# Optimization experiments

Measured on AMD Instinct MI355X. Metric: run time of the kernel, lower is better.

The kernel has to match this reference:

```python
import jax, jax.numpy as jnp
import numpy as np

BOX_W, GIOU_W, OBJ_W, CLS_W, CTR_W = 5.0, 2.0, 1.0, 1.5, 0.5
POS_RADIUS = 1.0


def _bce_logits(x, t):
    # numerically stable binary cross entropy with logits
    return jnp.maximum(x, 0.0) - x * t + jnp.log1p(jnp.exp(-jnp.abs(x)))


def _focal(logits, targets, alpha=0.25, gamma=2.0):
    p = jax.nn.sigmoid(logits)
    ce = _bce_logits(logits, targets)
    p_t = p * targets + (1.0 - p) * (1.0 - targets)
    a_t = alpha * targets + (1.0 - alpha) * (1.0 - targets)
    return (a_t * ce * (1.0 - p_t) ** gamma).mean()


def _centerness(ltrb):
    l, t, r, b = ltrb[..., 0], ltrb[..., 1], ltrb[..., 2], ltrb[..., 3]
    hor = jnp.minimum(l, r) / jnp.maximum(jnp.maximum(l, r), 1e-6)
    ver = jnp.minimum(t, b) / jnp.maximum(jnp.maximum(t, b), 1e-6)
    return jnp.sqrt(jnp.maximum(hor * ver, 0.0))


def _build_targets(locations, gt_boxes, gt_labels, grid_h, grid_w, num_classes):
    # Vectorized equivalent of the sequential smallest-area-first assignment:
    # each location takes the smallest-area gt among its candidate gts.
    lx, ly = locations[:, 0], locations[:, 1]            # [L]
    cx, cy, w, h = (gt_boxes[..., i] for i in range(4))  # [B,M]
    x1, y1, x2, y2 = cx - w / 2, cy - h / 2, cx + w / 2, cy + h / 2
    area = w * h                                          # [B,M]
    # [B,M,L] booleans
    inside_box = (lx > x1[..., None]) & (ly > y1[..., None]) & (lx < x2[..., None]) & (ly < y2[..., None])
    rx, ry = POS_RADIUS / grid_w, POS_RADIUS / grid_h
    inside_center = (jnp.abs(lx - cx[..., None]) <= rx) & (jnp.abs(ly - cy[..., None]) <= ry)
    candidate = inside_box & inside_center
    # fallback: objects with no candidate grab the closest location (prefer inside-box)
    dist = (lx - cx[..., None]) ** 2 + (ly - cy[..., None]) ** 2
    dist_in = jnp.where(inside_box, dist, jnp.inf)
    best = jnp.where(inside_box.any(-1), jnp.argmin(dist_in, -1), jnp.argmin(dist, -1))  # [B,M]
    L = lx.shape[0]
    fallback = jax.nn.one_hot(best, L, dtype=bool)
    candidate = jnp.where(candidate.any(-1, keepdims=True), candidate, fallback)
    # per-location: pick candidate gt with min area (first index on ties)
    cost = jnp.where(candidate, area[..., None], jnp.inf)   # [B,M,L]
    assigned = jnp.argmin(cost, axis=1)                      # [B,L]
    positive = jnp.isfinite(jnp.min(cost, axis=1))           # [B,L]
    gt_xyxy = jnp.stack([x1, y1, x2, y2], axis=-1)           # [B,M,4]
    abox = jnp.take_along_axis(gt_xyxy, assigned[:, :, None], axis=1)  # [B,L,4]
    ltrb = jnp.stack([lx - abox[..., 0], ly - abox[..., 1], abox[..., 2] - lx, abox[..., 3] - ly], axis=-1)
    ltrb = jnp.maximum(ltrb, 1e-6)
    pos_f = positive.astype(jnp.float32)
    alab = jnp.take_along_axis(gt_labels, assigned, axis=1)  # [B,L]
    cls_t = jax.nn.one_hot(alab, num_classes, dtype=jnp.float32) * pos_f[..., None]
    ctr_t = _centerness(ltrb) * pos_f
    return abox * pos_f[..., None], ltrb * pos_f[..., None], cls_t, pos_f, ctr_t, positive


def _detection_loss(boxes_xyxy, box_deltas, class_logits, objectness, centerness,
                    locations, gt_boxes, gt_labels, grid_h, grid_w):
    C = class_logits.shape[-1]
    box_t, ltrb_t, cls_t, obj_t, ctr_t, positive = _build_targets(
        locations, gt_boxes, gt_labels, grid_h, grid_w, C)
    loss_obj = _focal(objectness, obj_t)
    loss_cls = _focal(class_logits, cls_t)
    # positive-weighted box terms (masked weighted sums over the full grid)
    weights = jnp.where(positive, jnp.maximum(jax.lax.stop_gradient(ctr_t), 0.1), 0.0)  # [B,L]
    wsum = weights.sum()
    # smooth L1 on ltrb deltas, beta=0.1
    beta = 0.1
    d = jnp.abs(box_deltas - ltrb_t)
    l1 = jnp.where(d < beta, 0.5 * d * d / beta, d - 0.5 * beta).mean(-1)  # [B,L]
    loss_l1 = (l1 * weights).sum() / wsum
    # elementwise GIoU between predicted and assigned gt xyxy boxes
    p, g = boxes_xyxy, box_t
    inter_lt = jnp.maximum(p[..., :2], g[..., :2])
    inter_rb = jnp.minimum(p[..., 2:], g[..., 2:])
    inter_wh = jnp.maximum(inter_rb - inter_lt, 0.0)
    inter = inter_wh[..., 0] * inter_wh[..., 1]
    area_p = jnp.maximum(p[..., 2] - p[..., 0], 0.0) * jnp.maximum(p[..., 3] - p[..., 1], 0.0)
    area_g = jnp.maximum(g[..., 2] - g[..., 0], 0.0) * jnp.maximum(g[..., 3] - g[..., 1], 0.0)
    union = area_p + area_g - inter
    iou = inter / jnp.maximum(union, 1e-6)
    hull_lt = jnp.minimum(p[..., :2], g[..., :2])
    hull_rb = jnp.maximum(p[..., 2:], g[..., 2:])
    hull_wh = jnp.maximum(hull_rb - hull_lt, 0.0)
    hull = hull_wh[..., 0] * hull_wh[..., 1]
    giou = iou - (hull - union) / jnp.maximum(hull, 1e-6)
    loss_giou = ((1.0 - giou) * weights).sum() / wsum
    ctr_bce = _bce_logits(centerness, ctr_t)
    loss_ctr = (ctr_bce * weights).sum() / wsum
    return (OBJ_W * loss_obj + CTR_W * loss_ctr + CLS_W * loss_cls
            + BOX_W * loss_l1 + GIOU_W * loss_giou)


def setup_inputs() -> dict:
    key = jax.random.key(0)
    ks = jax.random.split(key, 8)
    B, M, H, W, C = 16, 32, 128, 128, 80
    L = H * W
    ys, xs = jnp.meshgrid(jnp.arange(H, dtype=jnp.float32), jnp.arange(W, dtype=jnp.float32), indexing='ij')
    locations = jnp.stack([(xs + 0.5) / W, (ys + 0.5) / H], axis=-1).reshape(L, 2)
    gt_c = jax.random.uniform(ks[0], (B, M, 2), minval=0.1, maxval=0.9)
    gt_wh = jax.random.uniform(ks[1], (B, M, 2), minval=0.02, maxval=0.3)
    gt_boxes = jnp.concatenate([gt_c, gt_wh], axis=-1)
    gt_labels = jax.random.randint(ks[2], (B, M), 0, C)
    pc = jax.random.uniform(ks[3], (B, L, 2), minval=0.05, maxval=0.95)
    pwh = jax.random.uniform(ks[4], (B, L, 2), minval=0.02, maxval=0.3)
    boxes_xyxy = jnp.concatenate([pc - pwh / 2, pc + pwh / 2], axis=-1)
    box_deltas = jax.random.uniform(ks[5], (B, L, 4), minval=1e-3, maxval=0.3)
    class_logits = jax.random.normal(ks[6], (B, L, C), dtype=jnp.float32)
    k7, k8 = jax.random.split(ks[7])
    objectness = jax.random.normal(k7, (B, L), dtype=jnp.float32)
    centerness = jax.random.normal(k8, (B, L), dtype=jnp.float32)
    return {"boxes_xyxy": boxes_xyxy, "box_deltas": box_deltas, "class_logits": class_logits,
            "objectness": objectness, "centerness": centerness, "locations": locations,
            "gt_boxes": gt_boxes, "gt_labels": gt_labels, "grid_h": H, "grid_w": W}


def reference(boxes_xyxy, box_deltas, class_logits, objectness, centerness,
              locations, gt_boxes, gt_labels, grid_h, grid_w):
    return _detection_loss(boxes_xyxy, box_deltas, class_logits, objectness, centerness,
                           locations, gt_boxes, gt_labels, grid_h, grid_w)
```

## Files before the change

### kernel.cpp

```cpp
#include <hip/hip_runtime.h>
#include <cstdint>
#include <cstddef>
#include <math.h>

#define BOX_W_C  5.0f
#define GIOU_W_C 2.0f
#define OBJ_W_C  1.0f
#define CLS_W_C  1.5f
#define CTR_W_C  0.5f
#define POS_RADIUS_C 1.0f
#define MAXM 128
#define CLS_BLOCKS 2048

__device__ __forceinline__ float focal_elem(float x, float t) {
    float ax = fabsf(x);
    float e  = __expf(-ax);
    float lg = __logf(1.0f + e);
    float ce = fmaxf(x, 0.0f) - x * t + lg;
    float p  = (x >= 0.0f) ? (1.0f / (1.0f + e)) : (e / (1.0f + e));
    float p_t = p * t + (1.0f - p) * (1.0f - t);
    float a_t = 0.25f * t + 0.75f * (1.0f - t);
    float om  = 1.0f - p_t;
    return a_t * ce * om * om;
}

__global__ void gt_assign_kernel(const float* __restrict__ locations,
                                 const float* __restrict__ gt_boxes,
                                 const int* __restrict__ gh_p,
                                 const int* __restrict__ gw_p,
                                 int L, int M,
                                 float* __restrict__ info,
                                 int* __restrict__ flags) {
    int bm  = blockIdx.x;
    int tid = threadIdx.x;

    const float* gb = gt_boxes + (size_t)bm * 4;
    float cx = gb[0], cy = gb[1], w = gb[2], h = gb[3];
    float x1 = cx - w * 0.5f, y1 = cy - h * 0.5f;
    float x2 = cx + w * 0.5f, y2 = cy + h * 0.5f;
    float area = w * h;
    float rx = POS_RADIUS_C / (float)gw_p[0];
    float ry = POS_RADIUS_C / (float)gh_p[0];

    float bin_v  = INFINITY; int bin_i  = 0x7fffffff;
    float ball_v = INFINITY; int ball_i = 0x7fffffff;
    int any_cand = 0, any_in = 0;

    const float2* loc2 = (const float2*)locations;
    for (int l = tid; l < L; l += blockDim.x) {
        float2 p2 = loc2[l];
        float lx = p2.x, ly = p2.y;
        bool inb = (lx > x1) && (ly > y1) && (lx < x2) && (ly < y2);
        bool inc = (fabsf(lx - cx) <= rx) && (fabsf(ly - cy) <= ry);
        any_cand |= (int)(inb && inc);
        any_in   |= (int)inb;
        float dx = lx - cx, dy = ly - cy;
        float dist = dx * dx + dy * dy;
        if (dist < ball_v) { ball_v = dist; ball_i = l; }
        float din = inb ? dist : INFINITY;
        if (din < bin_v) { bin_v = din; bin_i = l; }
    }

    __shared__ float s_v1[512]; __shared__ int s_i1[512];
    __shared__ float s_v2[512]; __shared__ int s_i2[512];
    __shared__ int s_c[512]; __shared__ int s_n[512];
    s_v1[tid] = bin_v;  s_i1[tid] = bin_i;
    s_v2[tid] = ball_v; s_i2[tid] = ball_i;
    s_c[tid] = any_cand; s_n[tid] = any_in;
    __syncthreads();
    for (int s = blockDim.x / 2; s > 0; s >>= 1) {
        if (tid < s) {
            if (s_v1[tid + s] < s_v1[tid] ||
                (s_v1[tid + s] == s_v1[tid] && s_i1[tid + s] < s_i1[tid])) {
                s_v1[tid] = s_v1[tid + s]; s_i1[tid] = s_i1[tid + s];
            }
            if (s_v2[tid + s] < s_v2[tid] ||
                (s_v2[tid + s] == s_v2[tid] && s_i2[tid + s] < s_i2[tid])) {
                s_v2[tid] = s_v2[tid + s]; s_i2[tid] = s_i2[tid + s];
            }
            s_c[tid] |= s_c[tid + s];
            s_n[tid] |= s_n[tid + s];
        }
        __syncthreads();
    }
    if (tid == 0) {
        int best = s_n[0] ? s_i1[0] : s_i2[0];
        flags[bm * 2]     = s_c[0];
        flags[bm * 2 + 1] = best;
        float* oi = info + (size_t)bm * 8;
        oi[0] = x1; oi[1] = y1; oi[2] = x2; oi[3] = y2;
        oi[4] = cx; oi[5] = cy; oi[6] = area; oi[7] = 0.0f;
    }
}

__global__ void assign_loss_kernel(const float* __restrict__ boxes_xyxy,
                                   const float* __restrict__ box_deltas,
                                   const float* __restrict__ objectness,
                                   const float* __restrict__ centerness,
                                   const float* __restrict__ locations,
                                   const int* __restrict__ gt_labels,
                                   const int* __restrict__ gh_p,
                                   const int* __restrict__ gw_p,
                                   int L, int M, int bpb, int nblk,
                                   const float* __restrict__ info,
                                   const int* __restrict__ flags,
                                   short* __restrict__ lab_out,
                                   float* __restrict__ partials) {
    __shared__ float s_x1[MAXM], s_y1[MAXM], s_x2[MAXM], s_y2[MAXM];
    __shared__ float s_cx[MAXM], s_cy[MAXM], s_area[MAXM];
    __shared__ int   s_lab[MAXM], s_hc[MAXM], s_best[MAXM];

    int b    = blockIdx.x / bpb;
    int lblk = blockIdx.x % bpb;
    int tid  = threadIdx.x;

    if (tid < M && tid < MAXM) {
        int bm = b * M + tid;
        const float* oi = info + (size_t)bm * 8;
        s_x1[tid] = oi[0]; s_y1[tid] = oi[1]; s_x2[tid] = oi[2]; s_y2[tid] = oi[3];
        s_cx[tid] = oi[4]; s_cy[tid] = oi[5]; s_area[tid] = oi[6];
        s_lab[tid]  = gt_labels[bm];
        s_hc[tid]   = flags[bm * 2];
        s_best[tid] = flags[bm * 2 + 1];
    }
    __syncthreads();

    int l = lblk * (int)blockDim.x + tid;
    float a_obj = 0.f, a_w = 0.f, a_l1 = 0.f, a_giou = 0.f, a_ctr = 0.f;

    if (l < L) {
        size_t bl = (size_t)b * L + l;
        const float2* loc2 = (const float2*)locations;
        float2 p2 = loc2[l];
        float lx = p2.x, ly = p2.y;
        float rx = POS_RADIUS_C / (float)gw_p[0];
        float ry = POS_RADIUS_C / (float)gh_p[0];

        float minc = INFINITY;
        int   asg  = -1;
        for (int m = 0; m < M; ++m) {
            bool cand;
            if (s_hc[m]) {
                cand = (lx > s_x1[m]) && (ly > s_y1[m]) && (lx < s_x2[m]) && (ly < s_y2[m])
                    && (fabsf(lx - s_cx[m]) <= rx) && (fabsf(ly - s_cy[m]) <= ry);
            } else {
                cand = (l == s_best[m]);
            }
            if (cand && (s_area[m] < minc)) { minc = s_area[m]; asg = m; }
        }
        bool  pos   = (asg >= 0);
        float pos_f = pos ? 1.0f : 0.0f;

        lab_out[bl] = pos ? (short)s_lab[asg] : (short)-1;

        a_obj = focal_elem(objectness[bl], pos_f);

        if (pos) {
            float ax1 = s_x1[asg], ay1 = s_y1[asg], ax2 = s_x2[asg], ay2 = s_y2[asg];
            float ltl = fmaxf(lx - ax1, 1e-6f);
            float ltt = fmaxf(ly - ay1, 1e-6f);
            float ltr = fmaxf(ax2 - lx, 1e-6f);
            float ltb = fmaxf(ay2 - ly, 1e-6f);
            float hor = fminf(ltl, ltr) / fmaxf(fmaxf(ltl, ltr), 1e-6f);
            float ver = fminf(ltt, ltb) / fmaxf(fmaxf(ltt, ltb), 1e-6f);
            float ctr_t = sqrtf(fmaxf(hor * ver, 0.0f));
            float wgt = fmaxf(ctr_t, 0.1f);
            a_w = wgt;

            const float4 bd = *(const float4*)(box_deltas + bl * 4);
            float d0 = fabsf(bd.x - ltl), d1 = fabsf(bd.y - ltt);
            float d2 = fabsf(bd.z - ltr), d3 = fabsf(bd.w - ltb);
            float l1s = ((d0 < 0.1f) ? (0.5f * d0 * d0 / 0.1f) : (d0 - 0.05f))
                      + ((d1 < 0.1f) ? (0.5f * d1 * d1 / 0.1f) : (d1 - 0.05f))
                      + ((d2 < 0.1f) ? (0.5f * d2 * d2 / 0.1f) : (d2 - 0.05f))
                      + ((d3 < 0.1f) ? (0.5f * d3 * d3 / 0.1f) : (d3 - 0.05f));
            a_l1 = (l1s * 0.25f) * wgt;

            const float4 pb = *(const float4*)(boxes_xyxy + bl * 4);
            float px1 = pb.x, py1 = pb.y, px2 = pb.z, py2 = pb.w;
            float ilx = fmaxf(px1, ax1), ily = fmaxf(py1, ay1);
            float irx = fminf(px2, ax2), iry = fminf(py2, ay2);
            float iw = fmaxf(irx - ilx, 0.f), ih = fmaxf(iry - ily, 0.f);
            float inter = iw * ih;
            float ap = fmaxf(px2 - px1, 0.f) * fmaxf(py2 - py1, 0.f);
            float ag = fmaxf(ax2 - ax1, 0.f) * fmaxf(ay2 - ay1, 0.f);
            float un = ap + ag - inter;
            float iou = inter / fmaxf(un, 1e-6f);
            float hlx = fminf(px1, ax1), hly = fminf(py1, ay1);
            float hrx = fmaxf(px2, ax2), hry = fmaxf(py2, ay2);
            float hw = fmaxf(hrx - hlx, 0.f), hh = fmaxf(hry - hly, 0.f);
            float hull = hw * hh;
            float giou = iou - (hull - un) / fmaxf(hull, 1e-6f);
            a_giou = (1.0f - giou) * wgt;

            float xc = centerness[bl];
            float bce = fmaxf(xc, 0.f) - xc * ctr_t + __logf(1.0f + __expf(-fabsf(xc)));
            a_ctr = bce * wgt;
        }
    }

    for (int off = 32; off > 0; off >>= 1) {
        a_obj  += __shfl_down(a_obj,  off);
        a_w    += __shfl_down(a_w,    off);
        a_l1   += __shfl_down(a_l1,   off);
        a_giou += __shfl_down(a_giou, off);
        a_ctr  += __shfl_down(a_ctr,  off);
    }
    __shared__ float red[4][5];
    int wid = tid >> 6;
    if ((tid & 63) == 0) {
        red[wid][0] = a_obj; red[wid][1] = a_w; red[wid][2] = a_l1;
        red[wid][3] = a_giou; red[wid][4] = a_ctr;
    }
    __syncthreads();
    if (tid == 0) {
        int nw = (int)blockDim.x >> 6;
        float r0 = 0.f, r1 = 0.f, r2 = 0.f, r3 = 0.f, r4 = 0.f;
        for (int w2 = 0; w2 < nw; ++w2) {
            r0 += red[w2][0]; r1 += red[w2][1]; r2 += red[w2][2];
            r3 += red[w2][3]; r4 += red[w2][4];
        }
        int blk = (int)blockIdx.x;
        partials[0 * nblk + blk] = r0;
        partials[1 * nblk + blk] = r1;
        partials[2 * nblk + blk] = r2;
        partials[3 * nblk + blk] = r3;
        partials[4 * nblk + blk] = r4;
    }
}

__global__ void cls_focal4_kernel(const float* __restrict__ class_logits,
                                  const short* __restrict__ lab,
                                  int total4, int C4,
                                  float* __restrict__ cls_partials) {
    const float4* cl4 = (const float4*)class_logits;
    int stride = (int)(gridDim.x * blockDim.x);
    float s = 0.f;
    for (int i = (int)(blockIdx.x * blockDim.x + threadIdx.x); i < total4; i += stride) {
        int loc = i / C4;
        int c0  = (i - loc * C4) << 2;
        int lv  = (int)lab[loc];
        float4 v = cl4[i];
        s += focal_elem(v.x, (c0     == lv) ? 1.f : 0.f);
        s += focal_elem(v.y, (c0 + 1 == lv) ? 1.f : 0.f);
        s += focal_elem(v.z, (c0 + 2 == lv) ? 1.f : 0.f);
        s += focal_elem(v.w, (c0 + 3 == lv) ? 1.f : 0.f);
    }
    for (int off = 32; off > 0; off >>= 1) s += __shfl_down(s, off);
    __shared__ float sw[4];
    int wid = threadIdx.x >> 6;
    if ((threadIdx.x & 63) == 0) sw[wid] = s;
    __syncthreads();
    if (threadIdx.x == 0) {
        int nw = (int)blockDim.x >> 6;
        float t = 0.f;
        for (int w2 = 0; w2 < nw; ++w2) t += sw[w2];
        cls_partials[blockIdx.x] = t;
    }
}

__global__ void cls_focal1_kernel(const float* __restrict__ class_logits,
                                  const short* __restrict__ lab,
                                  long total, int C,
                                  float* __restrict__ cls_partials) {
    long stride = (long)gridDim.x * blockDim.x;
    float s = 0.f;
    for (long i = (long)blockIdx.x * blockDim.x + threadIdx.x; i < total; i += stride) {
        long loc = i / C;
        int c = (int)(i - loc * C);
        int lv = (int)lab[loc];
        s += focal_elem(class_logits[i], (c == lv) ? 1.f : 0.f);
    }
    for (int off = 32; off > 0; off >>= 1) s += __shfl_down(s, off);
    __shared__ float sw[4];
    int wid = threadIdx.x >> 6;
    if ((threadIdx.x & 63) == 0) sw[wid] = s;
    __syncthreads();
    if (threadIdx.x == 0) {
        int nw = (int)blockDim.x >> 6;
        float t = 0.f;
        for (int w2 = 0; w2 < nw; ++w2) t += sw[w2];
        cls_partials[blockIdx.x] = t;
    }
}

__global__ void finalize_kernel(const float* __restrict__ partials, int nblk,
                                const float* __restrict__ cls_partials, int ncls,
                                float* __restrict__ out,
                                float invBL, float invBLC) {
    int tid = threadIdx.x;
    float r[5] = {0.f, 0.f, 0.f, 0.f, 0.f};
    for (int i = tid; i < nblk; i += blockDim.x) {
        r[0] += partials[0 * nblk + i];
        r[1] += partials[1 * nblk + i];
        r[2] += partials[2 * nblk + i];
        r[3] += partials[3 * nblk + i];
        r[4] += partials[4 * nblk + i];
    }
    float rc = 0.f;
    for (int i = tid; i < ncls; i += blockDim.x) rc += cls_partials[i];

    __shared__ float red[256][6];
    red[tid][0] = r[0]; red[tid][1] = r[1]; red[tid][2] = r[2];
    red[tid][3] = r[3]; red[tid][4] = r[4]; red[tid][5] = rc;
    __syncthreads();
    for (int s = (int)blockDim.x / 2; s > 0; s >>= 1) {
        if (tid < s) {
            for (int j = 0; j < 6; ++j) red[tid][j] += red[tid + s][j];
        }
        __syncthreads();
    }
    if (tid == 0) {
        float obj  = red[0][0] * invBL;
        float wsum = red[0][1];
        float l1   = red[0][2] / wsum;
        float giou = red[0][3] / wsum;
        float ctr  = red[0][4] / wsum;
        float cls  = red[0][5] * invBLC;
        out[0] = OBJ_W_C * obj + CTR_W_C * ctr + CLS_W_C * cls + BOX_W_C * l1 + GIOU_W_C * giou;
    }
}

extern "C" void kernel_launch(void* const* d_in, const int* in_sizes, int n_in,
                              void* d_out, int out_size, void* d_ws, size_t ws_size,
                              hipStream_t stream) {
    const float* boxes_xyxy   = (const float*)d_in[0];
    const float* box_deltas   = (const float*)d_in[1];
    const float* class_logits = (const float*)d_in[2];
    const float* objectness   = (const float*)d_in[3];
    const float* centerness   = (const float*)d_in[4];
    const float* locations    = (const float*)d_in[5];
    const float* gt_boxes     = (const float*)d_in[6];
    const int*   gt_labels    = (const int*)d_in[7];
    const int*   gh           = (const int*)d_in[8];
    const int*   gw           = (const int*)d_in[9];

    int L = in_sizes[5] / 2;
    int B = in_sizes[3] / L;
    int C = in_sizes[2] / in_sizes[3];
    int M = in_sizes[7] / B;

    int bpb  = (L + 255) / 256;
    int nblk = B * bpb;

    char* p = (char*)d_ws;
    short* lab    = (short*)p;            p += ((size_t)B * L * sizeof(short) + 63) / 64 * 64;
    int*   flags  = (int*)p;              p += ((size_t)B * M * 2 * sizeof(int) + 63) / 64 * 64;
    float* info   = (float*)p;            p += ((size_t)B * M * 8 * sizeof(float) + 63) / 64 * 64;
    float* partials = (float*)p;          p += ((size_t)5 * nblk * sizeof(float) + 63) / 64 * 64;
    float* cls_partials = (float*)p;

    gt_assign_kernel<<<B * M, 512, 0, stream>>>(locations, gt_boxes, gh, gw,
                                                L, M, info, flags);

    assign_loss_kernel<<<nblk, 256, 0, stream>>>(boxes_xyxy, box_deltas,
                                                 objectness, centerness,
                                                 locations, gt_labels, gh, gw,
                                                 L, M, bpb, nblk, info, flags,
                                                 lab, partials);

    size_t total = (size_t)B * L * C;
    int ncls;
    if ((C & 3) == 0 && total / 4 <= 0x7fffffff) {
        int total4 = (int)(total / 4);
        ncls = (total4 + 255) / 256;
        if (ncls > CLS_BLOCKS) ncls = CLS_BLOCKS;
        cls_focal4_kernel<<<ncls, 256, 0, stream>>>(class_logits, lab,
                                                    total4, C >> 2, cls_partials);
    } else {
        ncls = CLS_BLOCKS;
        cls_focal1_kernel<<<ncls, 256, 0, stream>>>(class_logits, lab,
                                                    (long)total, C, cls_partials);
    }

    float invBL  = (float)(1.0 / ((double)B * (double)L));
    float invBLC = (float)(1.0 / ((double)B * (double)L * (double)C));
    finalize_kernel<<<1, 256, 0, stream>>>(partials, nblk, cls_partials, ncls,
                                           (float*)d_out, invBL, invBLC);
}
```

Before: 181.6 us.

## Fuse class focal loss into per-location assignment kernel via shared labels

Merges the classification focal-loss pass into the assignment/loss kernel, so each block computes its 256 locations' labels into shared memory and then streams the matching class_logits rows. This removes the global label buffer write/read, one kernel launch, and the separate cls partials reduction. In exchange, the class-logit work is now tied to the assignment grid (one block per 256 locations), which may give less parallelism or worse load balance than the previous grid-stride kernel with up to 2048 blocks.

```diff
diff --git a/kernel.cpp b/kernel.cpp
--- a/kernel.cpp
+++ b/kernel.cpp
@@ -10,7 +10,7 @@
 #define CTR_W_C  0.5f
 #define POS_RADIUS_C 1.0f
 #define MAXM 128
-#define CLS_BLOCKS 2048
+#define BLK 256
 
 __device__ __forceinline__ float focal_elem(float x, float t) {
     float ax = fabsf(x);
@@ -93,22 +93,23 @@
     }
 }
 
-__global__ void assign_loss_kernel(const float* __restrict__ boxes_xyxy,
-                                   const float* __restrict__ box_deltas,
-                                   const float* __restrict__ objectness,
-                                   const float* __restrict__ centerness,
-                                   const float* __restrict__ locations,
-                                   const int* __restrict__ gt_labels,
-                                   const int* __restrict__ gh_p,
-                                   const int* __restrict__ gw_p,
-                                   int L, int M, int bpb, int nblk,
-                                   const float* __restrict__ info,
-                                   const int* __restrict__ flags,
-                                   short* __restrict__ lab_out,
-                                   float* __restrict__ partials) {
+__global__ void fused_loss_kernel(const float* __restrict__ boxes_xyxy,
+                                  const float* __restrict__ box_deltas,
+                                  const float* __restrict__ class_logits,
+                                  const float* __restrict__ objectness,
+                                  const float* __restrict__ centerness,
+                                  const float* __restrict__ locations,
+                                  const int* __restrict__ gt_labels,
+                                  const int* __restrict__ gh_p,
+                                  const int* __restrict__ gw_p,
+                                  int L, int M, int C, int bpb, int nblk,
+                                  const float* __restrict__ info,
+                                  const int* __restrict__ flags,
+                                  float* __restrict__ partials) {
     __shared__ float s_x1[MAXM], s_y1[MAXM], s_x2[MAXM], s_y2[MAXM];
     __shared__ float s_cx[MAXM], s_cy[MAXM], s_area[MAXM];
     __shared__ int   s_lab[MAXM], s_hc[MAXM], s_best[MAXM];
+    __shared__ int   s_loclab[BLK];
 
     int b    = blockIdx.x / bpb;
     int lblk = blockIdx.x % bpb;
@@ -125,8 +126,10 @@
     }
     __syncthreads();
 
-    int l = lblk * (int)blockDim.x + tid;
+    int l0 = lblk * BLK;
+    int l  = l0 + tid;
     float a_obj = 0.f, a_w = 0.f, a_l1 = 0.f, a_giou = 0.f, a_ctr = 0.f;
+    int mylab = -1;
 
     if (l < L) {
         size_t bl = (size_t)b * L + l;
@@ -150,8 +153,7 @@
         }
         bool  pos   = (asg >= 0);
         float pos_f = pos ? 1.0f : 0.0f;
-
-        lab_out[bl] = pos ? (short)s_lab[asg] : (short)-1;
+        mylab = pos ? s_lab[asg] : -1;
 
         a_obj = focal_elem(objectness[bl], pos_f);
 
@@ -198,6 +200,36 @@
             a_ctr = bce * wgt;
         }
     }
+    s_loclab[tid] = mylab;
+    __syncthreads();
+
+    float a_cls = 0.f;
+    int nrows = L - l0; if (nrows > BLK) nrows = BLK;
+    int C4 = C >> 2;
+    if (C4 > 0) {
+        const float4* cl4 = (const float4*)(class_logits + ((size_t)b * L + l0) * C);
+        int total_l = nrows * C4;
+        int q  = tid / C4;
+        int r  = tid - q * C4;
+        int dq = BLK / C4, dr = BLK - dq * C4;
+        for (int it = tid; it < total_l; it += BLK) {
+            int lv = s_loclab[q];
+            float4 v = cl4[it];
+            int c0 = r << 2;
+            a_cls += focal_elem(v.x, (c0     == lv) ? 1.f : 0.f);
+            a_cls += focal_elem(v.y, (c0 + 1 == lv) ? 1.f : 0.f);
+            a_cls += focal_elem(v.z, (c0 + 2 == lv) ? 1.f : 0.f);
+            a_cls += focal_elem(v.w, (c0 + 3 == lv) ? 1.f : 0.f);
+            q += dq; r += dr;
+            if (r >= C4) { ++q; r -= C4; }
+        }
+    }
+    int crem = C - (C4 << 2);
+    if (crem && l < L) {
+        const float* rowp = class_logits + ((size_t)b * L + l) * C + (C4 << 2);
+        for (int j = 0; j < crem; ++j)
+            a_cls += focal_elem(rowp[j], ((C4 << 2) + j == mylab) ? 1.f : 0.f);
+    }
 
     for (int off = 32; off > 0; off >>= 1) {
         a_obj  += __shfl_down(a_obj,  off);
@@ -205,20 +237,20 @@
         a_l1   += __shfl_down(a_l1,   off);
         a_giou += __shfl_down(a_giou, off);
         a_ctr  += __shfl_down(a_ctr,  off);
-    }
-    __shared__ float red[4][5];
+        a_cls  += __shfl_down(a_cls,  off);
+    }
+    __shared__ float red[BLK / 64][6];
     int wid = tid >> 6;
     if ((tid & 63) == 0) {
         red[wid][0] = a_obj; red[wid][1] = a_w; red[wid][2] = a_l1;
-        red[wid][3] = a_giou; red[wid][4] = a_ctr;
+        red[wid][3] = a_giou; red[wid][4] = a_ctr; red[wid][5] = a_cls;
     }
     __syncthreads();
     if (tid == 0) {
-        int nw = (int)blockDim.x >> 6;
-        float r0 = 0.f, r1 = 0.f, r2 = 0.f, r3 = 0.f, r4 = 0.f;
-        for (int w2 = 0; w2 < nw; ++w2) {
+        float r0 = 0.f, r1 = 0.f, r2 = 0.f, r3 = 0.f, r4 = 0.f, r5 = 0.f;
+        for (int w2 = 0; w2 < BLK / 64; ++w2) {
             r0 += red[w2][0]; r1 += red[w2][1]; r2 += red[w2][2];
-            r3 += red[w2][3]; r4 += red[w2][4];
+            r3 += red[w2][3]; r4 += red[w2][4]; r5 += red[w2][5];
         }
         int blk = (int)blockIdx.x;
         partials[0 * nblk + blk] = r0;
@@ -226,83 +258,25 @@
         partials[2 * nblk + blk] = r2;
         partials[3 * nblk + blk] = r3;
         partials[4 * nblk + blk] = r4;
-    }
-}
-
-__global__ void cls_focal4_kernel(const float* __restrict__ class_logits,
-                                  const short* __restrict__ lab,
-                                  int total4, int C4,
-                                  float* __restrict__ cls_partials) {
-    const float4* cl4 = (const float4*)class_logits;
-    int stride = (int)(gridDim.x * blockDim.x);
-    float s = 0.f;
-    for (int i = (int)(blockIdx.x * blockDim.x + threadIdx.x); i < total4; i += stride) {
-        int loc = i / C4;
-        int c0  = (i - loc * C4) << 2;
-        int lv  = (int)lab[loc];
-        float4 v = cl4[i];
-        s += focal_elem(v.x, (c0     == lv) ? 1.f : 0.f);
-        s += focal_elem(v.y, (c0 + 1 == lv) ? 1.f : 0.f);
-        s += focal_elem(v.z, (c0 + 2 == lv) ? 1.f : 0.f);
-        s += focal_elem(v.w, (c0 + 3 == lv) ? 1.f : 0.f);
-    }
-    for (int off = 32; off > 0; off >>= 1) s += __shfl_down(s, off);
-    __shared__ float sw[4];
-    int wid = threadIdx.x >> 6;
-    if ((threadIdx.x & 63) == 0) sw[wid] = s;
-    __syncthreads();
-    if (threadIdx.x == 0) {
-        int nw = (int)blockDim.x >> 6;
-        float t = 0.f;
-        for (int w2 = 0; w2 < nw; ++w2) t += sw[w2];
-        cls_partials[blockIdx.x] = t;
-    }
-}
-
-__global__ void cls_focal1_kernel(const float* __restrict__ class_logits,
-                                  const short* __restrict__ lab,
-                                  long total, int C,
-                                  float* __restrict__ cls_partials) {
-    long stride = (long)gridDim.x * blockDim.x;
-    float s = 0.f;
-    for (long i = (long)blockIdx.x * blockDim.x + threadIdx.x; i < total; i += stride) {
-        long loc = i / C;
-        int c = (int)(i - loc * C);
-        int lv = (int)lab[loc];
-        s += focal_elem(class_logits[i], (c == lv) ? 1.f : 0.f);
-    }
-    for (int off = 32; off > 0; off >>= 1) s += __shfl_down(s, off);
-    __shared__ float sw[4];
-    int wid = threadIdx.x >> 6;
-    if ((threadIdx.x & 63) == 0) sw[wid] = s;
-    __syncthreads();
-    if (threadIdx.x == 0) {
-        int nw = (int)blockDim.x >> 6;
-        float t = 0.f;
-        for (int w2 = 0; w2 < nw; ++w2) t += sw[w2];
-        cls_partials[blockIdx.x] = t;
+        partials[5 * nblk + blk] = r5;
     }
 }
 
 __global__ void finalize_kernel(const float* __restrict__ partials, int nblk,
-                                const float* __restrict__ cls_partials, int ncls,
                                 float* __restrict__ out,
                                 float invBL, float invBLC) {
     int tid = threadIdx.x;
-    float r[5] = {0.f, 0.f, 0.f, 0.f, 0.f};
+    float r[6] = {0.f, 0.f, 0.f, 0.f, 0.f, 0.f};
     for (int i = tid; i < nblk; i += blockDim.x) {
         r[0] += partials[0 * nblk + i];
         r[1] += partials[1 * nblk + i];
         r[2] += partials[2 * nblk + i];
         r[3] += partials[3 * nblk + i];
         r[4] += partials[4 * nblk + i];
-    }
-    float rc = 0.f;
-    for (int i = tid; i < ncls; i += blockDim.x) rc += cls_partials[i];
-
+        r[5] += partials[5 * nblk + i];
+    }
     __shared__ float red[256][6];
-    red[tid][0] = r[0]; red[tid][1] = r[1]; red[tid][2] = r[2];
-    red[tid][3] = r[3]; red[tid][4] = r[4]; red[tid][5] = rc;
+    for (int j = 0; j < 6; ++j) red[tid][j] = r[j];
     __syncthreads();
     for (int s = (int)blockDim.x / 2; s > 0; s >>= 1) {
         if (tid < s) {
@@ -340,41 +314,26 @@
     int C = in_sizes[2] / in_sizes[3];
     int M = in_sizes[7] / B;
 
-    int bpb  = (L + 255) / 256;
+    int bpb  = (L + BLK - 1) / BLK;
     int nblk = B * bpb;
 
     char* p = (char*)d_ws;
-    short* lab    = (short*)p;            p += ((size_t)B * L * sizeof(short) + 63) / 64 * 64;
     int*   flags  = (int*)p;              p += ((size_t)B * M * 2 * sizeof(int) + 63) / 64 * 64;
     float* info   = (float*)p;            p += ((size_t)B * M * 8 * sizeof(float) + 63) / 64 * 64;
-    float* partials = (float*)p;          p += ((size_t)5 * nblk * sizeof(float) + 63) / 64 * 64;
-    float* cls_partials = (float*)p;
+    float* partials = (float*)p;
 
     gt_assign_kernel<<<B * M, 512, 0, stream>>>(locations, gt_boxes, gh, gw,
                                                 L, M, info, flags);
 
-    assign_loss_kernel<<<nblk, 256, 0, stream>>>(boxes_xyxy, box_deltas,
-                                                 objectness, centerness,
-                                                 locations, gt_labels, gh, gw,
-                                                 L, M, bpb, nblk, info, flags,
-                                                 lab, partials);
-
-    size_t total = (size_t)B * L * C;
-    int ncls;
-    if ((C & 3) == 0 && total / 4 <= 0x7fffffff) {
-        int total4 = (int)(total / 4);
-        ncls = (total4 + 255) / 256;
-        if (ncls > CLS_BLOCKS) ncls = CLS_BLOCKS;
-        cls_focal4_kernel<<<ncls, 256, 0, stream>>>(class_logits, lab,
-                                                    total4, C >> 2, cls_partials);
-    } else {
-        ncls = CLS_BLOCKS;
-        cls_focal1_kernel<<<ncls, 256, 0, stream>>>(class_logits, lab,
-                                                    (long)total, C, cls_partials);
-    }
+    fused_loss_kernel<<<nblk, BLK, 0, stream>>>(boxes_xyxy, box_deltas,
+                                                class_logits, objectness,
+                                                centerness, locations,
+                                                gt_labels, gh, gw,
+                                                L, M, C, bpb, nblk,
+                                                info, flags, partials);
 
     float invBL  = (float)(1.0 / ((double)B * (double)L));
     float invBLC = (float)(1.0 / ((double)B * (double)L * (double)C));
-    finalize_kernel<<<1, 256, 0, stream>>>(partials, nblk, cls_partials, ncls,
-                                           (float*)d_out, invBL, invBLC);
-}
+    finalize_kernel<<<1, 256, 0, stream>>>(partials, nblk, (float*)d_out,
+                                           invBL, invBLC);
+}
```

New measurement: 179.7 us. Within noise of the previous version (-1.1%).
